# Optimization experiments

Measured on AMD Instinct MI355X. Metric: run time of the kernel, lower is better.

The kernel has to match this reference:

```python
import jax, jax.numpy as jnp
import numpy as np

BN_EPS = 1e-5
CURVE_LENGTH = 8

def _gumbel_st(logits):
    # straight-through gumbel-softmax (no gumbel noise, temperature=1), over last dim
    y = jax.nn.softmax(logits, axis=-1)
    ind = jnp.argmax(y, axis=-1)
    y_hard = jax.nn.one_hot(ind, logits.shape[-1], dtype=y.dtype)
    return jax.lax.stop_gradient(y_hard - y) + y

def _crossover(cur_vec, nb):
    # cur_vec: (B, c), nb: (B, c, k) -> clamp(1 + cosine, 0, 1), detached
    cur_vec = jax.lax.stop_gradient(cur_vec)
    nb = jax.lax.stop_gradient(nb)
    dot = jnp.einsum('bc,bck->bk', cur_vec, nb)
    n1 = jnp.linalg.norm(cur_vec, axis=1, keepdims=True)        # (B, 1)
    n2 = jnp.linalg.norm(nb, axis=1)                            # (B, k)
    cos = dot / jnp.maximum(n1 * n2, 1e-8)
    return jnp.clip(1.0 + cos, 0.0, 1.0)

def walk_forward(x, adj, cur, agent_w, agent_gamma, agent_beta, agent_mean, agent_var,
                 mom_w, mom_gamma, mom_beta, mom_mean, mom_var):
    bn, c, tot = x.shape
    k = adj.shape[-1]
    cn = cur.shape[1]
    flatten_x = jnp.transpose(x, (0, 2, 1)).reshape(bn * tot, c)
    offset = (jnp.arange(bn, dtype=adj.dtype) * tot)[:, None, None]
    tmp_adj = (adj + offset).reshape(bn * tot, k)
    flatten_cur = (cur + offset).reshape(-1)                    # (bn*cn,)
    inv_agent = agent_gamma / jnp.sqrt(agent_var + BN_EPS)      # (1,)
    inv_mom = mom_gamma / jnp.sqrt(mom_var + BN_EPS)            # (2,)
    rows = jnp.arange(bn * cn)
    curves = []
    pre_feature = cur_feature = cur_feature_cos = pre_feature_cos = None
    for step in range(CURVE_LENGTH):
        if step == 0:
            pre_feature = jnp.transpose(flatten_x[flatten_cur].reshape(bn, cn, c, 1), (0, 2, 1, 3))  # (bn,c,cn,1)
        else:
            cat1 = jnp.concatenate([cur_feature[..., 0], pre_feature[..., 0]], axis=1)  # (bn,2c,cn)
            mlog = jnp.einsum('bcn,oc->bon', cat1, mom_w)
            mlog = (mlog - mom_mean[None, :, None]) * inv_mom[None, :, None] + mom_beta[None, :, None]
            att = jax.nn.softmax(mlog, axis=1).reshape(bn, 1, cn, 2)  # faithful to torch .view
            cat2 = jnp.concatenate([cur_feature, pre_feature], axis=-1)  # (bn,c,cn,2)
            pre_feature = jnp.sum(cat2 * att, axis=-1, keepdims=True)    # (bn,c,cn,1)
            pre_feature_cos = jnp.transpose(pre_feature, (0, 2, 1, 3)).reshape(bn * cn, c)
        pick_idx = tmp_adj[flatten_cur]                                  # (bn*cn, k)
        pv_flat = flatten_x[pick_idx.reshape(-1)].reshape(bn * cn, k, c)
        pv_cos = jnp.transpose(pv_flat, (0, 2, 1))                       # (bn*cn, c, k)
        pick_values = jnp.transpose(pv_flat.reshape(bn, cn, k, c), (0, 3, 1, 2))  # (bn,c,cn,k)
        cat3 = jnp.concatenate([pick_values, jnp.broadcast_to(pre_feature, pick_values.shape)], axis=1)  # (bn,2c,cn,k)
        logits = jnp.einsum('bcnk,c->bnk', cat3, agent_w)[:, None]       # conv2d 1x1 -> (bn,1,cn,k)
        logits = (logits - agent_mean[0]) * inv_agent[0] + agent_beta[0]
        if step != 0:
            d = _crossover(cur_feature_cos - pre_feature_cos, pv_cos - cur_feature_cos[..., None])
            logits = logits * d.reshape(bn, cn, k)[:, None]
        sel = _gumbel_st(logits)                                         # (bn,1,cn,k)
        cur_feature = jnp.sum(pick_values * sel, axis=-1, keepdims=True)  # (bn,c,cn,1)
        cur_feature_cos = jnp.transpose(cur_feature, (0, 2, 1, 3)).reshape(bn * cn, c)
        cur_idx = jnp.argmax(sel, axis=-1).reshape(-1)                   # (bn*cn,)
        flatten_cur = pick_idx[rows, cur_idx]
        curves.append(cur_feature)
    return jnp.concatenate(curves, axis=-1)  # (bn, c, cn, curve_length)

def setup_inputs() -> dict:
    key = jax.random.key(0)
    ks = jax.random.split(key, 12)
    bn, c, tot, k, cn = 16, 64, 8192, 20, 512
    xyz = jax.random.normal(ks[0], (bn, 3, tot), dtype=jnp.float32)
    x = jax.random.normal(ks[1], (bn, c, tot), dtype=jnp.float32)
    adj = jax.random.randint(ks[2], (bn, tot, k), 0, tot)
    cur = jax.random.randint(ks[3], (bn, cn, 1), 0, tot)
    sc = 1.0 / np.sqrt(2 * c)
    agent_w = jax.random.normal(ks[4], (2 * c,), dtype=jnp.float32) * sc
    mom_w = jax.random.normal(ks[5], (2, 2 * c), dtype=jnp.float32) * sc
    agent_gamma = 1.0 + 0.1 * jax.random.normal(ks[6], (1,), dtype=jnp.float32)
    agent_beta = 0.1 * jax.random.normal(ks[7], (1,), dtype=jnp.float32)
    agent_mean = 0.1 * jax.random.normal(ks[8], (1,), dtype=jnp.float32)
    agent_var = jax.random.uniform(ks[9], (1,), minval=0.5, maxval=1.5, dtype=jnp.float32)
    mom_gamma = 1.0 + 0.1 * jax.random.normal(ks[10], (2,), dtype=jnp.float32)
    mom_beta = 0.1 * jax.random.normal(ks[11], (2,), dtype=jnp.float32)
    mom_mean = 0.1 * jax.random.normal(jax.random.fold_in(key, 101), (2,), dtype=jnp.float32)
    mom_var = jax.random.uniform(jax.random.fold_in(key, 102), (2,), minval=0.5, maxval=1.5, dtype=jnp.float32)
    return {"xyz": xyz, "x": x, "adj": adj, "cur": cur,
            "agent_w": agent_w, "agent_gamma": agent_gamma, "agent_beta": agent_beta,
            "agent_mean": agent_mean, "agent_var": agent_var,
            "mom_w": mom_w, "mom_gamma": mom_gamma, "mom_beta": mom_beta,
            "mom_mean": mom_mean, "mom_var": mom_var}

def reference(xyz, x, adj, cur, agent_w, agent_gamma, agent_beta, agent_mean, agent_var,
              mom_w, mom_gamma, mom_beta, mom_mean, mom_var):
    # xyz is accepted (as in the torch forward) but never used: the original code
    # calls `xyz.transpose(1, 2).contiguous` without invoking it.
    return walk_forward(x, adj, cur, agent_w, agent_gamma, agent_beta, agent_mean,
                        agent_var, mom_w, mom_gamma, mom_beta, mom_mean, mom_var)
```

## Files before the change

kernel.cpp:

```cpp
#include <hip/hip_runtime.h>
#include <cmath>

#define BN 16
#define CDIM 64
#define TOT 8192
#define KNB 20
#define CN 512
#define NSTEPS 8
#define WPB 16
#define BPB 32
#define WSTRIDE 577
#define LINE 32
#define MAGIC 0x5A17ECE1u
#define POISON 0xAAAAAAAAu

typedef float vf4 __attribute__((ext_vector_type(4)));

__device__ __forceinline__ float dot4(float a, float b, float c, float d,
                                      float wa, float wb, float wc, float wd) {
  return a * wa + b * wb + c * wc + d * wd;
}

template <int CTRL>
__device__ __forceinline__ float dpp_add(float v) {
  int o = __builtin_amdgcn_update_dpp(0, __float_as_int(v), CTRL, 0xF, 0xF, true);
  return v + __int_as_float(o);
}

__device__ __forceinline__ float gred16(float v) {
  v = dpp_add<0xB1>(v);
  v = dpp_add<0x4E>(v);
  v = dpp_add<0x141>(v);
  v = dpp_add<0x140>(v);
  return v;
}

__global__ __launch_bounds__(256, 2) void walk_kernel(
    const float* __restrict__ x, const int* __restrict__ adj, const int* __restrict__ cur,
    const float* __restrict__ agent_w, const float* __restrict__ agent_gamma,
    const float* __restrict__ agent_beta, const float* __restrict__ agent_mean,
    const float* __restrict__ agent_var, const float* __restrict__ mom_w,
    const float* __restrict__ mom_gamma, const float* __restrict__ mom_beta,
    const float* __restrict__ mom_mean, const float* __restrict__ mom_var,
    float* __restrict__ xt, float* __restrict__ pa,
    float* __restrict__ out, float* __restrict__ sbuf,
    unsigned int* __restrict__ pflag) {
  __shared__ float lds_out[WPB * WSTRIDE];
  const int tid  = threadIdx.x;
  const int lane = tid & 63;
  const int wv   = tid >> 6;
  const int g    = lane >> 4;
  const int L    = lane & 15;
  const int b     = (blockIdx.x & 7) + (((blockIdx.x >> 8) & 1) << 3);
  const int chunk = (blockIdx.x >> 3) & 31;
  const int w     = wv * 4 + g;
  const int n     = chunk * WPB + w;
  const int c0    = L << 2;
  const int mbase = (n << 2) & 1023;
  const int moff  = (n >= 256) ? 1 : 0;

  {
    float (*tile)[65] = (float (*)[65])lds_out;
#pragma unroll 1
    for (int i = 0; i < 4; ++i) {
      const int t0 = ((chunk << 2) + i) << 6;
#pragma unroll
      for (int k = 0; k < 4; ++k) {
        int fid = tid + k * 256;
        int cc = fid >> 4, qt = (fid & 15) << 2;
        float4 vv = *(const float4*)(x + ((size_t)b * CDIM + cc) * TOT + t0 + qt);
        tile[cc][qt + 0] = vv.x; tile[cc][qt + 1] = vv.y;
        tile[cc][qt + 2] = vv.z; tile[cc][qt + 3] = vv.w;
      }
      __syncthreads();
#pragma unroll
      for (int k = 0; k < 4; ++k) {
        int fid = tid + k * 256;
        int tt = fid >> 4, qc = (fid & 15) << 2;
        vf4 vv = {tile[qc + 0][tt], tile[qc + 1][tt], tile[qc + 2][tt], tile[qc + 3][tt]};
        float* dst = xt + ((size_t)b * TOT + t0 + tt) * CDIM + qc;
        asm volatile("global_store_dwordx4 %0, %1, off sc0 sc1" :: "v"(dst), "v"(vv) : "memory");
      }
      if (tid < 64) {
        const int tt = tid;
        float q[16];
#pragma unroll
        for (int l = 0; l < 16; ++l)
          q[l] = dot4(tile[4 * l][tt], tile[4 * l + 1][tt],
                      tile[4 * l + 2][tt], tile[4 * l + 3][tt],
                      agent_w[4 * l], agent_w[4 * l + 1],
                      agent_w[4 * l + 2], agent_w[4 * l + 3]);
        float sA = (q[0] + q[1]) + (q[2] + q[3]);
        float sB = (q[4] + q[5]) + (q[6] + q[7]);
        float sC = (q[8] + q[9]) + (q[10] + q[11]);
        float sD = (q[12] + q[13]) + (q[14] + q[15]);
        __hip_atomic_store(pa + (size_t)b * TOT + t0 + tt, (sA + sB) + (sC + sD),
                           __ATOMIC_RELAXED, __HIP_MEMORY_SCOPE_AGENT);
      }
      __syncthreads();
    }
    asm volatile("s_waitcnt vmcnt(0)" ::: "memory");
    __builtin_amdgcn_s_barrier();
    if (tid == 0)
      __hip_atomic_store(pflag + ((size_t)b * BPB + chunk) * LINE, MAGIC,
                         __ATOMIC_RELAXED, __HIP_MEMORY_SCOPE_AGENT);
    if (tid < BPB) {
      const unsigned int* f = pflag + ((size_t)b * BPB + tid) * LINE;
      while (__hip_atomic_load(f, __ATOMIC_RELAXED, __HIP_MEMORY_SCOPE_AGENT) != MAGIC)
        __builtin_amdgcn_s_sleep(2);
    }
    __builtin_amdgcn_s_barrier();
    asm volatile("" ::: "memory");
  }

  const vf4 aw2  = *(const vf4*)(agent_w + 64 + c0);
  const vf4 mw0a = *(const vf4*)(mom_w + c0);
  const vf4 mw0b = *(const vf4*)(mom_w + 64 + c0);
  const vf4 mw1a = *(const vf4*)(mom_w + 128 + c0);
  const vf4 mw1b = *(const vf4*)(mom_w + 192 + c0);
  const float amean  = agent_mean[0];
  const float abeta  = agent_beta[0];
  const float ainv   = agent_gamma[0] / sqrtf(agent_var[0] + 1e-5f);
  const float m0mean = mom_mean[0], m1mean = mom_mean[1];
  const float m0inv  = mom_gamma[0] / sqrtf(mom_var[0] + 1e-5f);
  const float m1inv  = mom_gamma[1] / sqrtf(mom_var[1] + 1e-5f);
  const float m0beta = mom_beta[0], m1beta = mom_beta[1];

  const float* xb   = xt + (size_t)b * TOT * CDIM;
  const float* pab  = pa + (size_t)b * TOT;
  const int*   adjb = adj + (size_t)b * TOT * KNB;
  float*       lout = lds_out + w * WSTRIDE;

  int t = cur[b * CN + n];
  vf4 pf = *(const vf4*)(xb + (size_t)t * CDIM + c0);
  vf4 cf = pf;
  vf4 u  = (vf4){0.f, 0.f, 0.f, 0.f};
  float A0v = 0.f, A1v = 0.f;

  int   idx[KNB];
  vf4   nv[KNB];
  float pav[KNB];
  float sq[KNB];
  {
    const int4* arow = (const int4*)(adjb + (size_t)t * KNB);
    int4 q0 = arow[0], q1 = arow[1], q2 = arow[2], q3 = arow[3], q4 = arow[4];
    int tmp[KNB] = {q0.x, q0.y, q0.z, q0.w, q1.x, q1.y, q1.z, q1.w,
                    q2.x, q2.y, q2.z, q2.w, q3.x, q3.y, q3.z, q3.w,
                    q4.x, q4.y, q4.z, q4.w};
#pragma unroll
    for (int j = 0; j < KNB; ++j) idx[j] = tmp[j];
#pragma unroll
    for (int j = 0; j < KNB; ++j) {
      nv[j]  = *(const vf4*)(xb + (size_t)idx[j] * CDIM + c0);
      pav[j] = pab[idx[j]];
    }
  }

#pragma unroll 1
  for (int s = 0; s < NSTEPS; ++s) {
    float n1 = 0.f;
    if (s > 0) {
      pf.x = A0v * cf.x + A1v * pf.x;
      pf.y = A0v * cf.y + A1v * pf.y;
      pf.z = A0v * cf.z + A1v * pf.z;
      pf.w = A0v * cf.w + A1v * pf.w;
      u.x = cf.x - pf.x; u.y = cf.y - pf.y; u.z = cf.z - pf.z; u.w = cf.w - pf.w;
      n1 = sqrtf(gred16(u.x * u.x + u.y * u.y + u.z * u.z + u.w * u.w));
    }
    float pw = gred16(pf.x * aw2.x + pf.y * aw2.y + pf.z * aw2.z + pf.w * aw2.w);

    float bestp = -3.4e38f;
    int   bestt = 0;
    vf4   bestv = (vf4){0.f, 0.f, 0.f, 0.f};
#pragma unroll
    for (int j = 0; j < KNB; ++j) {
      const vf4 v = nv[j];
      float logit = (pav[j] + pw - amean) * ainv + abeta;
      float p;
      if (s > 0) {
        float tx = v.x - cf.x, ty = v.y - cf.y, tz = v.z - cf.z, tw = v.w - cf.w;
        float su = tx * u.x + ty * u.y + tz * u.z + tw * u.w;
        su = gred16(su);
        float den  = fmaxf(n1 * sq[j], 1e-8f);
        float cosv = su * __builtin_amdgcn_rcpf(den);
        float dfac = fminf(fmaxf(1.0f + cosv, 0.0f), 1.0f);
        p = logit * dfac;
      } else {
        p = logit;
      }
      if (p > bestp) { bestp = p; bestt = idx[j]; bestv = v; }
    }
    cf = bestv;
    t  = bestt;
    lout[(c0 + 0) * 9 + s] = cf.x;
    lout[(c0 + 1) * 9 + s] = cf.y;
    lout[(c0 + 2) * 9 + s] = cf.z;
    lout[(c0 + 3) * 9 + s] = cf.w;

    if (s < NSTEPS - 1) {
      float p0 = cf.x * mw0a.x + cf.y * mw0a.y + cf.z * mw0a.z + cf.w * mw0a.w +
                 pf.x * mw0b.x + pf.y * mw0b.y + pf.z * mw0b.z + pf.w * mw0b.w;
      float p1 = cf.x * mw1a.x + cf.y * mw1a.y + cf.z * mw1a.z + cf.w * mw1a.w +
                 pf.x * mw1b.x + pf.y * mw1b.y + pf.z * mw1b.z + pf.w * mw1b.w;
      p0 = gred16(p0);
      p1 = gred16(p1);
      float mlog0 = (p0 - m0mean) * m0inv + m0beta;
      float mlog1 = (p1 - m1mean) * m1inv + m1beta;
      float mx = fmaxf(mlog0, mlog1);
      float e0 = expf(mlog0 - mx), e1 = expf(mlog1 - mx);
      float sinv = 1.0f / (e0 + e1);
      float* sb = sbuf + ((size_t)(b * NSTEPS + s + 1) << 10);
      if (L == 0) {
        unsigned long long pk =
            (unsigned long long)__float_as_uint(e0 * sinv) |
            ((unsigned long long)__float_as_uint(e1 * sinv) << 32);
        __hip_atomic_store((unsigned long long*)sb + n, pk,
                           __ATOMIC_RELAXED, __HIP_MEMORY_SCOPE_AGENT);
      }
      const int4* arow = (const int4*)(adjb + (size_t)t * KNB);
      int4 q0 = arow[0], q1 = arow[1], q2 = arow[2], q3 = arow[3], q4 = arow[4];
      int tmp[KNB] = {q0.x, q0.y, q0.z, q0.w, q1.x, q1.y, q1.z, q1.w,
                      q2.x, q2.y, q2.z, q2.w, q3.x, q3.y, q3.z, q3.w,
                      q4.x, q4.y, q4.z, q4.w};
#pragma unroll
      for (int j = 0; j < KNB; ++j) idx[j] = tmp[j];
#pragma unroll
      for (int j = 0; j < KNB; ++j) {
        nv[j]  = *(const vf4*)(xb + (size_t)idx[j] * CDIM + c0);
        pav[j] = pab[idx[j]];
      }
#pragma unroll
      for (int j = 0; j < KNB; ++j) {
        const vf4 v = nv[j];
        float tx = v.x - cf.x, ty = v.y - cf.y, tz = v.z - cf.z, tw = v.w - cf.w;
        float sn = tx * tx + ty * ty + tz * tz + tw * tw;
        sq[j] = sqrtf(gred16(sn));
      }
      {
        const unsigned* sbw = (const unsigned*)sb;
        const unsigned* q0p = sbw + mbase + moff;
        const unsigned* q2p = q0p + 2;
        unsigned w0, w2;
        for (;;) {
          w0 = __hip_atomic_load(q0p, __ATOMIC_RELAXED, __HIP_MEMORY_SCOPE_AGENT);
          w2 = __hip_atomic_load(q2p, __ATOMIC_RELAXED, __HIP_MEMORY_SCOPE_AGENT);
          if (w0 != POISON && w2 != POISON) break;
          __builtin_amdgcn_s_sleep(1);
        }
        A0v = __uint_as_float(w0);
        A1v = __uint_as_float(w2);
      }
      asm volatile("" ::: "memory");
    }
  }

#pragma unroll
  for (int e = 0; e < 4; ++e) {
    const float* src = lout + (c0 + e) * 9;
    float4 w0 = make_float4(src[0], src[1], src[2], src[3]);
    float4 w1 = make_float4(src[4], src[5], src[6], src[7]);
    float* op = out + (((size_t)(b * CDIM + c0 + e) * CN) + n) * NSTEPS;
    *(float4*)(op)     = w0;
    *(float4*)(op + 4) = w1;
  }
}

extern "C" void kernel_launch(void* const* d_in, const int* in_sizes, int n_in,
                              void* d_out, int out_size, void* d_ws, size_t ws_size,
                              hipStream_t stream) {
  (void)in_sizes; (void)n_in; (void)out_size; (void)ws_size;
  const float* x          = (const float*)d_in[1];
  const int*   adj        = (const int*)d_in[2];
  const int*   cur        = (const int*)d_in[3];
  const float* agent_w    = (const float*)d_in[4];
  const float* agent_gamma= (const float*)d_in[5];
  const float* agent_beta = (const float*)d_in[6];
  const float* agent_mean = (const float*)d_in[7];
  const float* agent_var  = (const float*)d_in[8];
  const float* mom_w      = (const float*)d_in[9];
  const float* mom_gamma  = (const float*)d_in[10];
  const float* mom_beta   = (const float*)d_in[11];
  const float* mom_mean   = (const float*)d_in[12];
  const float* mom_var    = (const float*)d_in[13];
  float* out = (float*)d_out;

  char* ws = (char*)d_ws;
  const size_t xt_bytes   = (size_t)BN * TOT * CDIM * sizeof(float);
  const size_t sbuf_bytes = (size_t)BN * NSTEPS * 2 * CN * sizeof(float);
  const size_t pa_bytes   = (size_t)BN * TOT * sizeof(float);
  float*        xt    = (float*)ws;
  float*        sbuf  = (float*)(ws + xt_bytes);
  float*        pab   = (float*)(ws + xt_bytes + sbuf_bytes);
  unsigned int* pflag = (unsigned int*)(ws + xt_bytes + sbuf_bytes + pa_bytes);

  walk_kernel<<<BN * BPB, 256, 0, stream>>>(x, adj, cur, agent_w, agent_gamma, agent_beta,
                                            agent_mean, agent_var, mom_w, mom_gamma, mom_beta,
                                            mom_mean, mom_var, xt, pab, out, sbuf, pflag);
}
```

Before: 162.5 us.

## Fuse agent projection into transpose, prefetch poll load, use 32-bit offsets, raise priority

Computes the per-point agent projection during the transpose store using a 16-lane DPP reduction, replacing the single-wave serial dot product. Issues the cross-block attention poll as one dwordx4 load early, so its latency overlaps the neighbor gathers. Also switches gather address math to 32-bit byte offsets, pre-scales pav by ainv to drop per-neighbor arithmetic, and raises wave priority during compute. These are several unrelated micro-optimizations; the early poll load may read stale data more often and need more retries.

```diff
diff --git a/kernel.cpp b/kernel.cpp
--- a/kernel.cpp
+++ b/kernel.cpp
@@ -15,6 +15,7 @@
 #define POISON 0xAAAAAAAAu
 
 typedef float vf4 __attribute__((ext_vector_type(4)));
+typedef unsigned uv4 __attribute__((ext_vector_type(4)));
 
 __device__ __forceinline__ float dot4(float a, float b, float c, float d,
                                       float wa, float wb, float wc, float wd) {
@@ -33,6 +34,13 @@
   v = dpp_add<0x141>(v);
   v = dpp_add<0x140>(v);
   return v;
+}
+
+__device__ __forceinline__ const vf4* vptr(const float* base, unsigned boff) {
+  return (const vf4*)((const char*)base + boff);
+}
+__device__ __forceinline__ float ldf(const float* base, unsigned boff) {
+  return *(const float*)((const char*)base + boff);
 }
 
 __global__ __launch_bounds__(256, 2) void walk_kernel(
@@ -57,10 +65,11 @@
   const int n     = chunk * WPB + w;
   const int c0    = L << 2;
   const int mbase = (n << 2) & 1023;
-  const int moff  = (n >= 256) ? 1 : 0;
+  const int moff  = (chunk >= 16) ? 1 : 0;
 
   {
     float (*tile)[65] = (float (*)[65])lds_out;
+    const vf4 awp = *(const vf4*)(agent_w + (L << 2));
 #pragma unroll 1
     for (int i = 0; i < 4; ++i) {
       const int t0 = ((chunk << 2) + i) << 6;
@@ -80,22 +89,10 @@
         vf4 vv = {tile[qc + 0][tt], tile[qc + 1][tt], tile[qc + 2][tt], tile[qc + 3][tt]};
         float* dst = xt + ((size_t)b * TOT + t0 + tt) * CDIM + qc;
         asm volatile("global_store_dwordx4 %0, %1, off sc0 sc1" :: "v"(dst), "v"(vv) : "memory");
-      }
-      if (tid < 64) {
-        const int tt = tid;
-        float q[16];
-#pragma unroll
-        for (int l = 0; l < 16; ++l)
-          q[l] = dot4(tile[4 * l][tt], tile[4 * l + 1][tt],
-                      tile[4 * l + 2][tt], tile[4 * l + 3][tt],
-                      agent_w[4 * l], agent_w[4 * l + 1],
-                      agent_w[4 * l + 2], agent_w[4 * l + 3]);
-        float sA = (q[0] + q[1]) + (q[2] + q[3]);
-        float sB = (q[4] + q[5]) + (q[6] + q[7]);
-        float sC = (q[8] + q[9]) + (q[10] + q[11]);
-        float sD = (q[12] + q[13]) + (q[14] + q[15]);
-        __hip_atomic_store(pa + (size_t)b * TOT + t0 + tt, (sA + sB) + (sC + sD),
-                           __ATOMIC_RELAXED, __HIP_MEMORY_SCOPE_AGENT);
+        float part = gred16(dot4(vv.x, vv.y, vv.z, vv.w, awp.x, awp.y, awp.z, awp.w));
+        if ((tid & 15) == 0)
+          __hip_atomic_store(pa + (size_t)b * TOT + t0 + tt, part,
+                             __ATOMIC_RELAXED, __HIP_MEMORY_SCOPE_AGENT);
       }
       __syncthreads();
     }
@@ -132,7 +129,7 @@
   float*       lout = lds_out + w * WSTRIDE;
 
   int t = cur[b * CN + n];
-  vf4 pf = *(const vf4*)(xb + (size_t)t * CDIM + c0);
+  vf4 pf = *vptr(xb, ((unsigned)t << 8) + (unsigned)(c0 << 2));
   vf4 cf = pf;
   vf4 u  = (vf4){0.f, 0.f, 0.f, 0.f};
   float A0v = 0.f, A1v = 0.f;
@@ -142,7 +139,7 @@
   float pav[KNB];
   float sq[KNB];
   {
-    const int4* arow = (const int4*)(adjb + (size_t)t * KNB);
+    const int4* arow = (const int4*)((const char*)adjb + (unsigned)t * 80u);
     int4 q0 = arow[0], q1 = arow[1], q2 = arow[2], q3 = arow[3], q4 = arow[4];
     int tmp[KNB] = {q0.x, q0.y, q0.z, q0.w, q1.x, q1.y, q1.z, q1.w,
                     q2.x, q2.y, q2.z, q2.w, q3.x, q3.y, q3.z, q3.w,
@@ -151,11 +148,12 @@
     for (int j = 0; j < KNB; ++j) idx[j] = tmp[j];
 #pragma unroll
     for (int j = 0; j < KNB; ++j) {
-      nv[j]  = *(const vf4*)(xb + (size_t)idx[j] * CDIM + c0);
-      pav[j] = pab[idx[j]];
+      nv[j]  = *vptr(xb, ((unsigned)idx[j] << 8) + (unsigned)(c0 << 2));
+      pav[j] = ldf(pab, (unsigned)idx[j] << 2) * ainv;
     }
   }
 
+  __builtin_amdgcn_s_setprio(1);
 #pragma unroll 1
   for (int s = 0; s < NSTEPS; ++s) {
     float n1 = 0.f;
@@ -168,6 +166,7 @@
       n1 = sqrtf(gred16(u.x * u.x + u.y * u.y + u.z * u.z + u.w * u.w));
     }
     float pw = gred16(pf.x * aw2.x + pf.y * aw2.y + pf.z * aw2.z + pf.w * aw2.w);
+    float lbase = (pw - amean) * ainv + abeta;
 
     float bestp = -3.4e38f;
     int   bestt = 0;
@@ -175,7 +174,7 @@
 #pragma unroll
     for (int j = 0; j < KNB; ++j) {
       const vf4 v = nv[j];
-      float logit = (pav[j] + pw - amean) * ainv + abeta;
+      float logit = pav[j] + lbase;
       float p;
       if (s > 0) {
         float tx = v.x - cf.x, ty = v.y - cf.y, tz = v.z - cf.z, tw = v.w - cf.w;
@@ -217,7 +216,12 @@
         __hip_atomic_store((unsigned long long*)sb + n, pk,
                            __ATOMIC_RELAXED, __HIP_MEMORY_SCOPE_AGENT);
       }
-      const int4* arow = (const int4*)(adjb + (size_t)t * KNB);
+      __builtin_amdgcn_s_setprio(0);
+      const char* pollp = (const char*)sb + ((unsigned)mbase << 2);
+      uv4 pr;
+      asm volatile("global_load_dwordx4 %0, %1, off sc0 sc1"
+                   : "=v"(pr) : "v"(pollp) : "memory");
+      const int4* arow = (const int4*)((const char*)adjb + (unsigned)t * 80u);
       int4 q0 = arow[0], q1 = arow[1], q2 = arow[2], q3 = arow[3], q4 = arow[4];
       int tmp[KNB] = {q0.x, q0.y, q0.z, q0.w, q1.x, q1.y, q1.z, q1.w,
                       q2.x, q2.y, q2.z, q2.w, q3.x, q3.y, q3.z, q3.w,
@@ -226,8 +230,8 @@
       for (int j = 0; j < KNB; ++j) idx[j] = tmp[j];
 #pragma unroll
       for (int j = 0; j < KNB; ++j) {
-        nv[j]  = *(const vf4*)(xb + (size_t)idx[j] * CDIM + c0);
-        pav[j] = pab[idx[j]];
+        nv[j]  = *vptr(xb, ((unsigned)idx[j] << 8) + (unsigned)(c0 << 2));
+        pav[j] = ldf(pab, (unsigned)idx[j] << 2) * ainv;
       }
 #pragma unroll
       for (int j = 0; j < KNB; ++j) {
@@ -237,19 +241,21 @@
         sq[j] = sqrtf(gred16(sn));
       }
       {
-        const unsigned* sbw = (const unsigned*)sb;
-        const unsigned* q0p = sbw + mbase + moff;
-        const unsigned* q2p = q0p + 2;
-        unsigned w0, w2;
-        for (;;) {
-          w0 = __hip_atomic_load(q0p, __ATOMIC_RELAXED, __HIP_MEMORY_SCOPE_AGENT);
-          w2 = __hip_atomic_load(q2p, __ATOMIC_RELAXED, __HIP_MEMORY_SCOPE_AGENT);
-          if (w0 != POISON && w2 != POISON) break;
+        asm volatile("s_waitcnt vmcnt(0)" ::: "memory");
+        unsigned w0 = moff ? pr.y : pr.x;
+        unsigned w2 = moff ? pr.w : pr.z;
+        while (w0 == POISON || w2 == POISON) {
           __builtin_amdgcn_s_sleep(1);
+          asm volatile("global_load_dwordx4 %0, %1, off sc0 sc1"
+                       : "=v"(pr) : "v"(pollp) : "memory");
+          asm volatile("s_waitcnt vmcnt(0)" ::: "memory");
+          w0 = moff ? pr.y : pr.x;
+          w2 = moff ? pr.w : pr.z;
         }
         A0v = __uint_as_float(w0);
         A1v = __uint_as_float(w2);
       }
+      __builtin_amdgcn_s_setprio(1);
       asm volatile("" ::: "memory");
     }
   }
```

Result: no change. 160.8 us (-1.1%).
